# Kernel optimization log

Hardware: AMD Instinct MI355X
Metric: run time of the kernel (lower is better)

Reference implementation:

```python
import jax, jax.numpy as jnp
import numpy as np

SUB = 5      # icosphere subdivisions -> V = 10*4^5 + 2 = 10242
B = 16       # batch size
ZD = 32      # z_dim
HID = 64     # hidden_dim


def _create_icosphere(sub):
    t = (1.0 + np.sqrt(5.0)) / 2.0
    v = np.array([[-1, t, 0], [1, t, 0], [-1, -t, 0], [1, -t, 0], [0, -1, t], [0, 1, t],
                  [0, -1, -t], [0, 1, -t], [t, 0, -1], [t, 0, 1], [-t, 0, -1], [-t, 0, 1]],
                 dtype=np.float32)
    v /= np.linalg.norm(v[0])
    f = np.array([[0, 11, 5], [0, 5, 1], [0, 1, 7], [0, 7, 10], [0, 10, 11], [1, 5, 9],
                  [5, 11, 4], [11, 10, 2], [10, 7, 6], [7, 1, 8], [3, 9, 4], [3, 4, 2],
                  [3, 2, 6], [3, 6, 8], [3, 8, 9], [4, 9, 5], [2, 4, 11], [6, 2, 10],
                  [8, 6, 7], [9, 8, 1]], dtype=np.int64)
    for _ in range(sub):
        mid = {}
        nv = list(v)
        nf = []
        def gm(i1, i2):
            k = (min(i1, i2), max(i1, i2))
            if k not in mid:
                m = (v[i1] + v[i2]) / 2.0
                m = m / np.linalg.norm(m)
                mid[k] = len(nv)
                nv.append(m)
            return mid[k]
        for v0, v1, v2 in f:
            a, b, c = gm(v0, v1), gm(v1, v2), gm(v2, v0)
            nf.extend([[v0, a, c], [v1, b, a], [v2, c, b], [a, b, c]])
        v = np.array(nv, dtype=np.float32)
        f = np.array(nf, dtype=np.int64)
    return v, f


def _adjacency(faces, nv):
    # symmetric edges + self loops, sym-normalized: 1/sqrt(deg[r]*deg[c])
    e = set()
    for a, b, c in faces:
        e.update([(int(a), int(b)), (int(b), int(a)), (int(b), int(c)),
                  (int(c), int(b)), (int(c), int(a)), (int(a), int(c))])
    for i in range(nv):
        e.add((i, i))
    e = np.array(sorted(e), dtype=np.int64)
    row, col = e[:, 0], e[:, 1]
    deg = np.bincount(row, minlength=nv).astype(np.float32)
    vals = (1.0 / np.sqrt(deg[row] * deg[col])).astype(np.float32)
    return row.astype(np.int32), col.astype(np.int32), vals


def _lin(key, din, dout):
    W = jax.random.normal(key, (dout, din), jnp.float32) / np.sqrt(din)
    b = jnp.zeros((dout,), jnp.float32)
    return W, b


def setup_inputs() -> dict:
    verts, faces = _create_icosphere(SUB)
    V = len(verts)
    row, col, vals = _adjacency(faces, V)
    template = jnp.asarray(verts)

    key = jax.random.key(0)
    ks = jax.random.split(key, 16)
    # input meshes = template + small deformation (realistic for this VAE)
    x = template[None] + 0.05 * jax.random.normal(ks[0], (B, V, 3), jnp.float32)
    eps = jax.random.normal(ks[1], (B, ZD), jnp.float32)

    W1, b1 = _lin(ks[2], 3, HID)
    W2, b2 = _lin(ks[3], HID, HID)
    W3, b3 = _lin(ks[4], HID, 2 * HID)
    Wfc, bfc = _lin(ks[5], 2 * HID, 4 * HID)
    Wmu, bmu = _lin(ks[6], 4 * HID, ZD)
    Wlv, blv = _lin(ks[7], 4 * HID, ZD)
    DH = 2 * HID  # decoder hidden_dim = 128
    Wd1, bd1 = _lin(ks[8], ZD + 3, DH)
    Wd2, bd2 = _lin(ks[9], DH, DH)
    Wd3, bd3 = _lin(ks[10], DH, DH // 2)
    Wd4, bd4 = _lin(ks[11], DH // 2, 3)

    return {"x": x, "eps": eps, "row": jnp.asarray(row), "col": jnp.asarray(col),
            "vals": jnp.asarray(vals), "template": template,
            "W1": W1, "b1": b1, "W2": W2, "b2": b2, "W3": W3, "b3": b3,
            "Wfc": Wfc, "bfc": bfc, "Wmu": Wmu, "bmu": bmu, "Wlv": Wlv, "blv": blv,
            "Wd1": Wd1, "bd1": bd1, "Wd2": Wd2, "bd2": bd2,
            "Wd3": Wd3, "bd3": bd3, "Wd4": Wd4, "bd4": bd4}


def _spmm(row, col, vals, h):
    # batched sparse (V,V) @ (B,V,C): out[b,r] = sum_e vals[e] * h[b, col[e]]
    msg = h[:, col, :] * vals[None, :, None]            # (B, E, C)
    return jnp.zeros(h.shape, h.dtype).at[:, row, :].add(msg)


def _linear(x, W, b):
    return x @ W.T + b


def reference(x, eps, row, col, vals, template,
              W1, b1, W2, b2, W3, b3, Wfc, bfc, Wmu, bmu, Wlv, blv,
              Wd1, bd1, Wd2, bd2, Wd3, bd3, Wd4, bd4):
    # --- encoder: 3 graph convs (linear -> spmm -> relu), mean pool, fc ---
    h = jax.nn.relu(_spmm(row, col, vals, _linear(x, W1, b1)))
    h = jax.nn.relu(_spmm(row, col, vals, _linear(h, W2, b2)))
    h = jax.nn.relu(_spmm(row, col, vals, _linear(h, W3, b3)))
    g = h.mean(axis=1)                                   # (B, 2*HID)
    feat = jax.nn.relu(_linear(g, Wfc, bfc))             # (B, 4*HID)
    mu = _linear(feat, Wmu, bmu)                         # (B, ZD)
    log_var = jnp.clip(_linear(feat, Wlv, blv), -20.0, 20.0)
    # --- reparameterize (eps supplied as input for determinism) ---
    z = mu + eps * jnp.exp(0.5 * log_var)
    # --- decoder MLP on [z, template] per vertex (dropout = eval mode) ---
    Bn, V = x.shape[0], template.shape[0]
    z_exp = jnp.broadcast_to(z[:, None, :], (Bn, V, z.shape[-1]))
    t_exp = jnp.broadcast_to(template[None], (Bn, V, 3))
    hd = jnp.concatenate([z_exp, t_exp], axis=-1)        # (B, V, ZD+3)
    hd = jax.nn.relu(_linear(hd, Wd1, bd1))
    hd = jax.nn.relu(_linear(hd, Wd2, bd2))
    hd = jax.nn.relu(_linear(hd, Wd3, bd3))
    offsets = _linear(hd, Wd4, bd4)                      # (B, V, 3)
    recon = template[None] + offsets
    return recon, mu, log_var
```

## Files before the change

### kernel.cpp

```cpp
#include <hip/hip_runtime.h>
#include <hip/hip_bf16.h>

typedef __attribute__((ext_vector_type(8))) unsigned short ushort8;
typedef __attribute__((ext_vector_type(4))) unsigned short ushort4v;
typedef __attribute__((ext_vector_type(8))) short short8v;
typedef __attribute__((ext_vector_type(4))) float f32x4;

__device__ __forceinline__ float bf2f(unsigned short u){
  union { unsigned int i; float f; } x; x.i = ((unsigned int)u) << 16; return x.f;
}
__device__ __forceinline__ unsigned short f2bf(float f){
  __hip_bfloat16 h = __float2bfloat16(f);
  return *reinterpret_cast<unsigned short*>(&h);
}

__device__ __forceinline__ void sw_decode(int p, int NB, int& b, int& off){
  int xcd = p & 7, q = p >> 3;
  int hi = (q >= NB) ? 1 : 0;
  b = xcd + (hi << 3);
  off = q - (hi ? NB : 0);
}

__global__ void prep_k(const int* __restrict__ row, const int* __restrict__ colx,
                       const float* __restrict__ vals, int nnz,
                       int* __restrict__ col8, float* __restrict__ val8,
                       float* __restrict__ dvec, float* __restrict__ g, int V, int GN){
  int v = blockIdx.x*256 + threadIdx.x;
  if (v < GN) g[v] = 0.f;
  if (v >= V) return;
  int lo = 0, hi = nnz;
  while (lo < hi){ int m = (lo+hi)>>1; if (row[m] < v) lo = m+1; else hi = m; }
  int e0 = lo;
  int lo2 = e0; hi = nnz;
  while (lo2 < hi){ int m = (lo2+hi)>>1; if (row[m] < v+1) lo2 = m+1; else hi = m; }
  int e1 = lo2;
  float s = 0.f;
  #pragma unroll
  for (int i=0;i<8;i++){
    int e = e0 + i;
    int c  = (e < e1) ? colx[e] : 0;
    float wv = (e < e1) ? vals[e] : 0.f;
    col8[v*8+i] = c; val8[v*8+i] = wv; s += wv;
  }
  dvec[v] = s;
}

__device__ __forceinline__ void load_nbr(const int* __restrict__ col8,
    const float* __restrict__ val8, int v, int* cols, float* vv){
  int4 ca = *reinterpret_cast<const int4*>(col8 + v*8);
  int4 cb = *reinterpret_cast<const int4*>(col8 + v*8 + 4);
  float4 va = *reinterpret_cast<const float4*>(val8 + v*8);
  float4 vb = *reinterpret_cast<const float4*>(val8 + v*8 + 4);
  cols[0]=ca.x; cols[1]=ca.y; cols[2]=ca.z; cols[3]=ca.w;
  cols[4]=cb.x; cols[5]=cb.y; cols[6]=cb.z;
  vv[0]=va.x; vv[1]=va.y; vv[2]=va.z; vv[3]=va.w;
  vv[4]=vb.x; vv[5]=vb.y; vv[6]=vb.z;
}

__global__ void spmm_lin1_k(const float* __restrict__ x, const int* __restrict__ col8,
    const float* __restrict__ val8, const float* __restrict__ d,
    const float* __restrict__ W1, const float* __restrict__ b1,
    unsigned short* __restrict__ out, int V, int NB){
  __shared__ float sW[192];
  __shared__ float sB[64];
  int tid = threadIdx.x;
  if (tid < 192) sW[tid] = W1[tid];
  if (tid < 64)  sB[tid] = b1[tid];
  __syncthreads();
  int b, off; sw_decode(blockIdx.x, NB, b, off);
  int v = off*256 + tid;
  if (v >= V) return;
  const float* xb = x + (size_t)b*V*3;
  int   cs[7]; float ws[7];
  load_nbr(col8, val8, v, cs, ws);
  float s0=0.f, s1=0.f, s2=0.f;
  #pragma unroll
  for (int i=0;i<7;i++){
    const float* xr = xb + (size_t)cs[i]*3;
    s0 += ws[i]*xr[0]; s1 += ws[i]*xr[1]; s2 += ws[i]*xr[2];
  }
  float dv = d[v];
  unsigned short* orow = out + ((size_t)b*V + v)*64;
  #pragma unroll
  for (int cg=0; cg<8; ++cg){
    ushort8 o;
    #pragma unroll
    for (int k=0;k<8;k++){
      int c = cg*8 + k;
      float acc = dv*sB[c] + s0*sW[c*3] + s1*sW[c*3+1] + s2*sW[c*3+2];
      o[k] = f2bf(fmaxf(acc, 0.f));
    }
    *reinterpret_cast<ushort8*>(orow + cg*8) = o;
  }
}

__global__ __launch_bounds__(256) void spmm8s_k(const unsigned short* __restrict__ in,
    unsigned short* __restrict__ out, const int* __restrict__ col8,
    const float* __restrict__ val8, int V, int NB){
  int b, off; sw_decode(blockIdx.x, NB, b, off);
  int j = off*256 + (int)threadIdx.x;
  if (j >= V*8) return;
  int cg = j & 7; int v = j >> 3;
  const unsigned short* base = in + (size_t)b*V*64 + cg*8;
  int cols[7]; float vv[7];
  load_nbr(col8, val8, v, cols, vv);
  ushort8 g[7];
  #pragma unroll
  for (int i=0;i<7;i++) g[i] = *reinterpret_cast<const ushort8*>(base + (size_t)cols[i]*64);
  float acc[8];
  #pragma unroll
  for (int k=0;k<8;k++) acc[k] = 0.f;
  #pragma unroll
  for (int i=0;i<7;i++){
    float s = vv[i];
    #pragma unroll
    for (int k=0;k<8;k++) acc[k] += s*bf2f(g[i][k]);
  }
  ushort8 o;
  #pragma unroll
  for (int k=0;k<8;k++) o[k] = f2bf(acc[k]);
  *reinterpret_cast<ushort8*>(out + ((size_t)b*V + v)*64 + cg*8) = o;
}

template<int K, int N, bool RELU>
__global__ __launch_bounds__(256) void lin_mfma_k(const unsigned short* __restrict__ in,
    const float* __restrict__ W, const float* __restrict__ bias,
    unsigned short* __restrict__ out, const float* __restrict__ dvec, int V, int NB){
  constexpr int KP = K + 8;
  constexpr int NF = N / 16;
  constexpr int KS = K / 32;
  __shared__ unsigned short sW[N * KP];
  __shared__ float sB[N];
  int tid = threadIdx.x;
  for (int i = tid*4; i < N*K; i += 1024){
    const float4 wv = *reinterpret_cast<const float4*>(W + i);
    int n = i / K, k = i - n*K;
    unsigned short* dst = &sW[n*KP + k];
    dst[0] = f2bf(wv.x); dst[1] = f2bf(wv.y); dst[2] = f2bf(wv.z); dst[3] = f2bf(wv.w);
  }
  if (tid < N) sB[tid] = bias[tid];
  __syncthreads();

  int b, off; sw_decode(blockIdx.x, NB, b, off);
  const int wave = tid >> 6, lane = tid & 63;
  const int l15 = lane & 15, lg = lane >> 4;
  const int vbase = off*128 + wave*32;

  int v0r = vbase + l15, v1r = vbase + 16 + l15;
  int v0c = min(v0r, V-1), v1c = min(v1r, V-1);
  const size_t bb = (size_t)b*V;
  const unsigned short* bp0 = in + (bb + v0c)*K + lg*8;
  const unsigned short* bp1 = in + (bb + v1c)*K + lg*8;
  const unsigned short* aBase = &sW[l15*KP + lg*8];

  f32x4 acc[NF][2];
  #pragma unroll
  for (int nf=0; nf<NF; ++nf){ acc[nf][0] = (f32x4)0.f; acc[nf][1] = (f32x4)0.f; }

  #pragma unroll
  for (int ks=0; ks<KS; ++ks){
    short8v b0 = *reinterpret_cast<const short8v*>(bp0 + ks*32);
    short8v b1 = *reinterpret_cast<const short8v*>(bp1 + ks*32);
    #pragma unroll
    for (int nf=0; nf<NF; ++nf){
      short8v a = *reinterpret_cast<const short8v*>(aBase + nf*16*KP + ks*32);
      acc[nf][0] = __builtin_amdgcn_mfma_f32_16x16x32_bf16(a, b0, acc[nf][0], 0,0,0);
      acc[nf][1] = __builtin_amdgcn_mfma_f32_16x16x32_bf16(a, b1, acc[nf][1], 0,0,0);
    }
  }

  float d0 = dvec[v0c], d1 = dvec[v1c];
  #pragma unroll
  for (int rr=0; rr<2; ++rr){
    int v = rr ? v1r : v0r;
    if (v >= V) continue;
    float ds = rr ? d1 : d0;
    #pragma unroll
    for (int nf=0; nf<NF; ++nf){
      int nb = nf*16 + lg*4;
      ushort4v o;
      #pragma unroll
      for (int reg=0; reg<4; ++reg){
        float val = acc[nf][rr][reg] + ds*sB[nb + reg];
        if (RELU) val = val > 0.f ? val : 0.f;
        o[reg] = f2bf(val);
      }
      *reinterpret_cast<ushort4v*>(out + (bb + v)*N + nb) = o;
    }
  }
}

__global__ __launch_bounds__(256) void lin3_mean_k(const unsigned short* __restrict__ in,
    const float* __restrict__ W, const float* __restrict__ bias,
    const float* __restrict__ dvec, float* __restrict__ g, int V, int NB){
  constexpr int K = 64, N = 128, KP = K + 8, NF = N/16, KS = K/32;
  __shared__ unsigned short sW[N * KP];
  __shared__ float sB[N];
  __shared__ float gPart[128];
  int tid = threadIdx.x;
  for (int i = tid*4; i < N*K; i += 1024){
    const float4 wv = *reinterpret_cast<const float4*>(W + i);
    int n = i / K, k = i - n*K;
    unsigned short* dst = &sW[n*KP + k];
    dst[0] = f2bf(wv.x); dst[1] = f2bf(wv.y); dst[2] = f2bf(wv.z); dst[3] = f2bf(wv.w);
  }
  if (tid < N) sB[tid] = bias[tid];
  if (tid < 128) gPart[tid] = 0.f;
  __syncthreads();

  int b, off; sw_decode(blockIdx.x, NB, b, off);
  const int wave = tid >> 6, lane = tid & 63;
  const int l15 = lane & 15, lg = lane >> 4;
  const int vbase = off*128 + wave*32;

  int v0r = vbase + l15, v1r = vbase + 16 + l15;
  int v0c = min(v0r, V-1), v1c = min(v1r, V-1);
  const size_t bb = (size_t)b*V;
  const unsigned short* bp0 = in + (bb + v0c)*K + lg*8;
  const unsigned short* bp1 = in + (bb + v1c)*K + lg*8;
  const unsigned short* aBase = &sW[l15*KP + lg*8];

  f32x4 acc[NF][2];
  #pragma unroll
  for (int nf=0; nf<NF; ++nf){ acc[nf][0] = (f32x4)0.f; acc[nf][1] = (f32x4)0.f; }

  #pragma unroll
  for (int ks=0; ks<KS; ++ks){
    short8v b0 = *reinterpret_cast<const short8v*>(bp0 + ks*32);
    short8v b1 = *reinterpret_cast<const short8v*>(bp1 + ks*32);
    #pragma unroll
    for (int nf=0; nf<NF; ++nf){
      short8v a = *reinterpret_cast<const short8v*>(aBase + nf*16*KP + ks*32);
      acc[nf][0] = __builtin_amdgcn_mfma_f32_16x16x32_bf16(a, b0, acc[nf][0], 0,0,0);
      acc[nf][1] = __builtin_amdgcn_mfma_f32_16x16x32_bf16(a, b1, acc[nf][1], 0,0,0);
    }
  }

  bool ok0 = v0r < V, ok1 = v1r < V;
  float d0 = dvec[v0c], d1 = dvec[v1c];
  #pragma unroll
  for (int nf=0; nf<NF; ++nf){
    #pragma unroll
    for (int reg=0; reg<4; ++reg){
      int c = nf*16 + lg*4 + reg;
      float v0f = fmaxf(acc[nf][0][reg] + d0*sB[c], 0.f);
      float v1f = fmaxf(acc[nf][1][reg] + d1*sB[c], 0.f);
      float sA = (ok0 ? v0f : 0.f) + (ok1 ? v1f : 0.f);
      #pragma unroll
      for (int m=1; m<16; m<<=1) sA += __shfl_xor(sA, m);
      if (l15 == 0) atomicAdd(&gPart[c], sA);
    }
  }
  __syncthreads();
  if (tid < 128){
    float a = gPart[tid];
    if (a != 0.f) atomicAdd(&g[b*128 + tid], a);
  }
}

__global__ __launch_bounds__(256) void head2_k(const float* __restrict__ g,
    const float* __restrict__ Wfc, const float* __restrict__ bfc,
    const float* __restrict__ Wmu, const float* __restrict__ bmu,
    const float* __restrict__ Wlv, const float* __restrict__ blv,
    const float* __restrict__ eps, const float* __restrict__ Wd1,
    const float* __restrict__ bd1, float* __restrict__ mu_out,
    float* __restrict__ lv_out, float* __restrict__ zp, float invV){
  int b = blockIdx.x;
  int tid = threadIdx.x;
  __shared__ float sG[128];
  __shared__ float sF[256];
  __shared__ float sMu[32];
  __shared__ float sLv[32];
  __shared__ float sZ[32];
  if (tid < 128) sG[tid] = g[b*128 + tid] * invV;
  __syncthreads();
  {
    const float4* wr = reinterpret_cast<const float4*>(Wfc + tid*128);
    float acc = bfc[tid];
    #pragma unroll 8
    for (int k4=0;k4<32;k4++){
      float4 wv = wr[k4];
      acc += sG[k4*4]*wv.x + sG[k4*4+1]*wv.y + sG[k4*4+2]*wv.z + sG[k4*4+3]*wv.w;
    }
    sF[tid] = fmaxf(acc, 0.f);
  }
  __syncthreads();
  if (tid < 64){
    int c = tid & 31;
    bool isMu = tid < 32;
    const float4* wr = reinterpret_cast<const float4*>((isMu ? Wmu : Wlv) + c*256);
    float acc = isMu ? bmu[c] : blv[c];
    #pragma unroll 8
    for (int k4=0;k4<64;k4++){
      float4 wv = wr[k4];
      acc += sF[k4*4]*wv.x + sF[k4*4+1]*wv.y + sF[k4*4+2]*wv.z + sF[k4*4+3]*wv.w;
    }
    if (isMu){ sMu[c] = acc; mu_out[b*32+c] = acc; }
    else {
      acc = fminf(20.f, fmaxf(-20.f, acc));
      sLv[c] = acc; lv_out[b*32+c] = acc;
    }
  }
  __syncthreads();
  if (tid < 32) sZ[tid] = sMu[tid] + eps[b*32+tid]*expf(0.5f*sLv[tid]);
  __syncthreads();
  if (tid < 128){
    const float* wr = Wd1 + tid*35;
    float acc = bd1[tid];
    #pragma unroll
    for (int k=0;k<32;k++) acc += sZ[k]*wr[k];
    zp[b*128 + tid] = acc;
  }
}

__global__ __launch_bounds__(256) void dec_k(const float* __restrict__ zp,
    const float* __restrict__ tmpl, const float* __restrict__ Wd1,
    const float* __restrict__ Wd2, const float* __restrict__ bd2,
    const float* __restrict__ Wd3, const float* __restrict__ bd3,
    const float* __restrict__ Wd4, const float* __restrict__ bd4,
    float* __restrict__ out, int V, int NB){
  constexpr int KP = 136;
  __shared__ unsigned short sW[64*KP];
  __shared__ unsigned short sH[64*KP];
  __shared__ float sB2[128];
  __shared__ float sB3[64];
  __shared__ float sW4[192];
  __shared__ float sB4[3];
  __shared__ float sZPb[128];
  __shared__ float sWT[128*3];
  int tid = threadIdx.x;
  int b, off; sw_decode(blockIdx.x, NB, b, off);

  if (tid < 128) sB2[tid] = bd2[tid];
  if (tid < 64)  sB3[tid] = bd3[tid];
  if (tid < 192) sW4[tid] = Wd4[tid];
  if (tid < 3)   sB4[tid] = bd4[tid];
  if (tid < 128) sZPb[tid] = zp[b*128 + tid];
  if (tid < 128){
    sWT[tid*3+0] = Wd1[tid*35+32];
    sWT[tid*3+1] = Wd1[tid*35+33];
    sWT[tid*3+2] = Wd1[tid*35+34];
  }
  auto stageW = [&](const float* Wsrc){
    for (int i = tid*4; i < 64*128; i += 1024){
      float4 wv = *reinterpret_cast<const float4*>(Wsrc + i);
      int n = i >> 7, k = i & 127;
      unsigned short* dst = &sW[n*KP + k];
      dst[0]=f2bf(wv.x); dst[1]=f2bf(wv.y); dst[2]=f2bf(wv.z); dst[3]=f2bf(wv.w);
    }
  };
  stageW(Wd2);
  __syncthreads();

  const int wave = tid >> 6, lane = tid & 63;
  const int l15 = lane & 15, lg = lane >> 4;
  const int vbase = off*64 + wave*16;
  const int lrow = wave*16;

  int v0r = vbase + l15;
  int v0 = min(v0r, V-1);
  float t0x=tmpl[v0*3], t0y=tmpl[v0*3+1], t0z=tmpl[v0*3+2];

  short8v bf0[4];
  #pragma unroll
  for (int ks=0; ks<4; ++ks){
    #pragma unroll
    for (int k=0;k<8;k++){
      int c = lg*8 + ks*32 + k;
      const float* wt = &sWT[c*3];
      bf0[ks][k] = (short)f2bf(fmaxf(sZPb[c] + t0x*wt[0]+t0y*wt[1]+t0z*wt[2], 0.f));
    }
  }

  const unsigned short* aBase = &sW[l15*KP + lg*8];

  #pragma unroll
  for (int half=0; half<2; ++half){
    if (half==1){
      __syncthreads();
      stageW(Wd2 + 64*128);
      __syncthreads();
    }
    f32x4 acc[4];
    #pragma unroll
    for (int nf=0; nf<4; ++nf) acc[nf]=(f32x4)0.f;
    #pragma unroll
    for (int ks=0; ks<4; ++ks){
      #pragma unroll
      for (int nf=0; nf<4; ++nf){
        short8v a = *reinterpret_cast<const short8v*>(aBase + nf*16*KP + ks*32);
        acc[nf] = __builtin_amdgcn_mfma_f32_16x16x32_bf16(a, bf0[ks], acc[nf], 0,0,0);
      }
    }
    #pragma unroll
    for (int nf=0; nf<4; ++nf){
      int c = half*64 + nf*16 + lg*4;
      ushort4v o;
      #pragma unroll
      for (int reg=0; reg<4; ++reg)
        o[reg] = f2bf(fmaxf(acc[nf][reg] + sB2[c+reg], 0.f));
      *reinterpret_cast<ushort4v*>(&sH[(lrow + l15)*KP + c]) = o;
    }
  }
  __syncthreads();
  stageW(Wd3);
  __syncthreads();

  f32x4 acc3[4];
  #pragma unroll
  for (int nf=0; nf<4; ++nf) acc3[nf]=(f32x4)0.f;
  #pragma unroll
  for (int ks=0; ks<4; ++ks){
    short8v h0 = *reinterpret_cast<const short8v*>(&sH[(lrow + l15)*KP + ks*32 + lg*8]);
    #pragma unroll
    for (int nf=0; nf<4; ++nf){
      short8v a = *reinterpret_cast<const short8v*>(aBase + nf*16*KP + ks*32);
      acc3[nf] = __builtin_amdgcn_mfma_f32_16x16x32_bf16(a, h0, acc3[nf], 0,0,0);
    }
  }

  float p0 = 0.f, p1 = 0.f, p2 = 0.f;
  #pragma unroll
  for (int nf=0; nf<4; ++nf){
    #pragma unroll
    for (int reg=0; reg<4; ++reg){
      int c = nf*16 + lg*4 + reg;
      float h = fmaxf(acc3[nf][reg] + sB3[c], 0.f);
      p0 += h*sW4[c]; p1 += h*sW4[64+c]; p2 += h*sW4[128+c];
    }
  }
  p0 += __shfl_xor(p0,16); p0 += __shfl_xor(p0,32);
  p1 += __shfl_xor(p1,16); p1 += __shfl_xor(p1,32);
  p2 += __shfl_xor(p2,16); p2 += __shfl_xor(p2,32);
  if (lg == 0 && v0r < V){
    size_t o = ((size_t)b*V + v0r)*3;
    out[o+0] = tmpl[v0r*3+0] + p0 + sB4[0];
    out[o+1] = tmpl[v0r*3+1] + p1 + sB4[1];
    out[o+2] = tmpl[v0r*3+2] + p2 + sB4[2];
  }
}

extern "C" void kernel_launch(void* const* d_in, const int* in_sizes, int n_in,
                              void* d_out, int out_size, void* d_ws, size_t ws_size,
                              hipStream_t stream){
  const float* x    = (const float*)d_in[0];
  const float* eps  = (const float*)d_in[1];
  const int*   row  = (const int*)d_in[2];
  const int*   colx = (const int*)d_in[3];
  const float* vals = (const float*)d_in[4];
  const float* tmpl = (const float*)d_in[5];
  const float* W1 = (const float*)d_in[6];  const float* b1 = (const float*)d_in[7];
  const float* W2 = (const float*)d_in[8];  const float* b2 = (const float*)d_in[9];
  const float* W3 = (const float*)d_in[10]; const float* b3 = (const float*)d_in[11];
  const float* Wfc= (const float*)d_in[12]; const float* bfc= (const float*)d_in[13];
  const float* Wmu= (const float*)d_in[14]; const float* bmu= (const float*)d_in[15];
  const float* Wlv= (const float*)d_in[16]; const float* blv= (const float*)d_in[17];
  const float* Wd1= (const float*)d_in[18]; const float* bd1= (const float*)d_in[19];
  const float* Wd2= (const float*)d_in[20]; const float* bd2= (const float*)d_in[21];
  const float* Wd3= (const float*)d_in[22]; const float* bd3= (const float*)d_in[23];
  const float* Wd4= (const float*)d_in[24]; const float* bd4= (const float*)d_in[25];

  int V   = in_sizes[5] / 3;
  int Bn  = in_sizes[1] / 32;
  int nnz = in_sizes[2];
  int R   = Bn * V;

  char* w = (char*)d_ws;
  size_t off = 0;
  auto alloc = [&](size_t bytes)->char*{
    char* p = w + off; off = (off + bytes + 255) & ~(size_t)255; return p;
  };
  unsigned short* bufA = (unsigned short*)alloc((size_t)R * 64 * 2);
  unsigned short* bufB = (unsigned short*)alloc((size_t)R * 64 * 2);
  int*   col8 = (int*)alloc((size_t)V*8*4);
  float* val8 = (float*)alloc((size_t)V*8*4);
  float* dvec = (float*)alloc((size_t)V*4);
  float* g    = (float*)alloc((size_t)Bn*128*4);
  float* zpb  = (float*)alloc((size_t)Bn*128*4);

  float* recon  = (float*)d_out;
  float* mu_out = recon + (size_t)R*3;
  float* lv_out = mu_out + (size_t)Bn*32;

  int NB1 = (V + 255) / 256;
  int NB8 = (V*8 + 255) / 256;
  int NBm = (V + 127) / 128;
  int NBd = (V + 63) / 64;

  prep_k<<<(V+255)/256, 256, 0, stream>>>(row, colx, vals, nnz, col8, val8, dvec, g, V, Bn*128);

  spmm_lin1_k<<<16*NB1, 256, 0, stream>>>(x, col8, val8, dvec, W1, b1, bufA, V, NB1);
  spmm8s_k<<<16*NB8, 256, 0, stream>>>(bufA, bufB, col8, val8, V, NB8);
  lin_mfma_k<64,64,true><<<16*NBm, 256, 0, stream>>>(bufB, W2, b2, bufA, dvec, V, NBm);
  spmm8s_k<<<16*NB8, 256, 0, stream>>>(bufA, bufB, col8, val8, V, NB8);
  lin3_mean_k<<<16*NBm, 256, 0, stream>>>(bufB, W3, b3, dvec, g, V, NBm);

  head2_k<<<Bn, 256, 0, stream>>>(g, Wfc, bfc, Wmu, bmu, Wlv, blv, eps, Wd1, bd1,
                                  mu_out, lv_out, zpb, 1.0f/(float)V);

  dec_k<<<16*NBd, 256, 0, stream>>>(zpb, tmpl, Wd1, Wd2, bd2, Wd3, bd3, Wd4, bd4,
                                    recon, V, NBd);
}
```

Before: 132.2 us.

## Make linear and decoder kernels persistent to amortize weight staging across tiles

Three kernels (lin_mfma, lin3_mean, dec) now run as grid-stride persistent kernels with 32 blocks per batch item instead of one block per tile. Each block converts and stages its weights into shared memory once and then loops over many vertex tiles. lin3_mean accumulates pooled sums in registers across tiles before doing one shuffle-reduce and atomic pass. The decoder keeps both Wd2 and Wd3 resident in LDS, which removes the per-tile restaging and syncs but raises shared memory use and may lower occupancy.

```diff
diff --git a/kernel.cpp b/kernel.cpp
--- a/kernel.cpp
+++ b/kernel.cpp
@@ -125,7 +125,8 @@
 template<int K, int N, bool RELU>
 __global__ __launch_bounds__(256) void lin_mfma_k(const unsigned short* __restrict__ in,
     const float* __restrict__ W, const float* __restrict__ bias,
-    unsigned short* __restrict__ out, const float* __restrict__ dvec, int V, int NB){
+    unsigned short* __restrict__ out, const float* __restrict__ dvec, int V,
+    int NBLK, int NT){
   constexpr int KP = K + 8;
   constexpr int NF = N / 16;
   constexpr int KS = K / 32;
@@ -141,58 +142,60 @@
   if (tid < N) sB[tid] = bias[tid];
   __syncthreads();
 
-  int b, off; sw_decode(blockIdx.x, NB, b, off);
-  const int wave = tid >> 6, lane = tid & 63;
+  int b, off0; sw_decode(blockIdx.x, NBLK, b, off0);
+  const int lane = tid & 63, wave = tid >> 6;
   const int l15 = lane & 15, lg = lane >> 4;
-  const int vbase = off*128 + wave*32;
-
-  int v0r = vbase + l15, v1r = vbase + 16 + l15;
-  int v0c = min(v0r, V-1), v1c = min(v1r, V-1);
   const size_t bb = (size_t)b*V;
-  const unsigned short* bp0 = in + (bb + v0c)*K + lg*8;
-  const unsigned short* bp1 = in + (bb + v1c)*K + lg*8;
   const unsigned short* aBase = &sW[l15*KP + lg*8];
 
-  f32x4 acc[NF][2];
-  #pragma unroll
-  for (int nf=0; nf<NF; ++nf){ acc[nf][0] = (f32x4)0.f; acc[nf][1] = (f32x4)0.f; }
-
-  #pragma unroll
-  for (int ks=0; ks<KS; ++ks){
-    short8v b0 = *reinterpret_cast<const short8v*>(bp0 + ks*32);
-    short8v b1 = *reinterpret_cast<const short8v*>(bp1 + ks*32);
-    #pragma unroll
-    for (int nf=0; nf<NF; ++nf){
-      short8v a = *reinterpret_cast<const short8v*>(aBase + nf*16*KP + ks*32);
-      acc[nf][0] = __builtin_amdgcn_mfma_f32_16x16x32_bf16(a, b0, acc[nf][0], 0,0,0);
-      acc[nf][1] = __builtin_amdgcn_mfma_f32_16x16x32_bf16(a, b1, acc[nf][1], 0,0,0);
-    }
-  }
-
-  float d0 = dvec[v0c], d1 = dvec[v1c];
-  #pragma unroll
-  for (int rr=0; rr<2; ++rr){
-    int v = rr ? v1r : v0r;
-    if (v >= V) continue;
-    float ds = rr ? d1 : d0;
-    #pragma unroll
-    for (int nf=0; nf<NF; ++nf){
-      int nb = nf*16 + lg*4;
-      ushort4v o;
-      #pragma unroll
-      for (int reg=0; reg<4; ++reg){
-        float val = acc[nf][rr][reg] + ds*sB[nb + reg];
-        if (RELU) val = val > 0.f ? val : 0.f;
-        o[reg] = f2bf(val);
-      }
-      *reinterpret_cast<ushort4v*>(out + (bb + v)*N + nb) = o;
+  for (int off = off0; off < NT; off += NBLK){
+    const int vbase = off*128 + wave*32;
+    int v0r = vbase + l15, v1r = vbase + 16 + l15;
+    int v0c = min(v0r, V-1), v1c = min(v1r, V-1);
+    const unsigned short* bp0 = in + (bb + v0c)*K + lg*8;
+    const unsigned short* bp1 = in + (bb + v1c)*K + lg*8;
+
+    f32x4 acc[NF][2];
+    #pragma unroll
+    for (int nf=0; nf<NF; ++nf){ acc[nf][0] = (f32x4)0.f; acc[nf][1] = (f32x4)0.f; }
+
+    #pragma unroll
+    for (int ks=0; ks<KS; ++ks){
+      short8v b0 = *reinterpret_cast<const short8v*>(bp0 + ks*32);
+      short8v b1 = *reinterpret_cast<const short8v*>(bp1 + ks*32);
+      #pragma unroll
+      for (int nf=0; nf<NF; ++nf){
+        short8v a = *reinterpret_cast<const short8v*>(aBase + nf*16*KP + ks*32);
+        acc[nf][0] = __builtin_amdgcn_mfma_f32_16x16x32_bf16(a, b0, acc[nf][0], 0,0,0);
+        acc[nf][1] = __builtin_amdgcn_mfma_f32_16x16x32_bf16(a, b1, acc[nf][1], 0,0,0);
+      }
+    }
+
+    float d0 = dvec[v0c], d1 = dvec[v1c];
+    #pragma unroll
+    for (int rr=0; rr<2; ++rr){
+      int v = rr ? v1r : v0r;
+      if (v >= V) continue;
+      float ds = rr ? d1 : d0;
+      #pragma unroll
+      for (int nf=0; nf<NF; ++nf){
+        int nb = nf*16 + lg*4;
+        ushort4v o;
+        #pragma unroll
+        for (int reg=0; reg<4; ++reg){
+          float val = acc[nf][rr][reg] + ds*sB[nb + reg];
+          if (RELU) val = val > 0.f ? val : 0.f;
+          o[reg] = f2bf(val);
+        }
+        *reinterpret_cast<ushort4v*>(out + (bb + v)*N + nb) = o;
+      }
     }
   }
 }
 
 __global__ __launch_bounds__(256) void lin3_mean_k(const unsigned short* __restrict__ in,
     const float* __restrict__ W, const float* __restrict__ bias,
-    const float* __restrict__ dvec, float* __restrict__ g, int V, int NB){
+    const float* __restrict__ dvec, float* __restrict__ g, int V, int NBLK, int NT){
   constexpr int K = 64, N = 128, KP = K + 8, NF = N/16, KS = K/32;
   __shared__ unsigned short sW[N * KP];
   __shared__ float sB[N];
@@ -208,44 +211,61 @@
   if (tid < 128) gPart[tid] = 0.f;
   __syncthreads();
 
-  int b, off; sw_decode(blockIdx.x, NB, b, off);
-  const int wave = tid >> 6, lane = tid & 63;
+  int b, off0; sw_decode(blockIdx.x, NBLK, b, off0);
+  const int lane = tid & 63, wave = tid >> 6;
   const int l15 = lane & 15, lg = lane >> 4;
-  const int vbase = off*128 + wave*32;
-
-  int v0r = vbase + l15, v1r = vbase + 16 + l15;
-  int v0c = min(v0r, V-1), v1c = min(v1r, V-1);
   const size_t bb = (size_t)b*V;
-  const unsigned short* bp0 = in + (bb + v0c)*K + lg*8;
-  const unsigned short* bp1 = in + (bb + v1c)*K + lg*8;
   const unsigned short* aBase = &sW[l15*KP + lg*8];
 
-  f32x4 acc[NF][2];
-  #pragma unroll
-  for (int nf=0; nf<NF; ++nf){ acc[nf][0] = (f32x4)0.f; acc[nf][1] = (f32x4)0.f; }
-
-  #pragma unroll
-  for (int ks=0; ks<KS; ++ks){
-    short8v b0 = *reinterpret_cast<const short8v*>(bp0 + ks*32);
-    short8v b1 = *reinterpret_cast<const short8v*>(bp1 + ks*32);
+  float racc[NF][4];
+  #pragma unroll
+  for (int nf=0;nf<NF;++nf)
+    #pragma unroll
+    for (int reg=0;reg<4;++reg) racc[nf][reg] = 0.f;
+
+  for (int off = off0; off < NT; off += NBLK){
+    const int vbase = off*128 + wave*32;
+    int v0r = vbase + l15, v1r = vbase + 16 + l15;
+    int v0c = min(v0r, V-1), v1c = min(v1r, V-1);
+    const unsigned short* bp0 = in + (bb + v0c)*K + lg*8;
+    const unsigned short* bp1 = in + (bb + v1c)*K + lg*8;
+
+    f32x4 acc[NF][2];
+    #pragma unroll
+    for (int nf=0; nf<NF; ++nf){ acc[nf][0] = (f32x4)0.f; acc[nf][1] = (f32x4)0.f; }
+
+    #pragma unroll
+    for (int ks=0; ks<KS; ++ks){
+      short8v b0 = *reinterpret_cast<const short8v*>(bp0 + ks*32);
+      short8v b1 = *reinterpret_cast<const short8v*>(bp1 + ks*32);
+      #pragma unroll
+      for (int nf=0; nf<NF; ++nf){
+        short8v a = *reinterpret_cast<const short8v*>(aBase + nf*16*KP + ks*32);
+        acc[nf][0] = __builtin_amdgcn_mfma_f32_16x16x32_bf16(a, b0, acc[nf][0], 0,0,0);
+        acc[nf][1] = __builtin_amdgcn_mfma_f32_16x16x32_bf16(a, b1, acc[nf][1], 0,0,0);
+      }
+    }
+
+    bool ok0 = v0r < V, ok1 = v1r < V;
+    float d0 = dvec[v0c], d1 = dvec[v1c];
     #pragma unroll
     for (int nf=0; nf<NF; ++nf){
-      short8v a = *reinterpret_cast<const short8v*>(aBase + nf*16*KP + ks*32);
-      acc[nf][0] = __builtin_amdgcn_mfma_f32_16x16x32_bf16(a, b0, acc[nf][0], 0,0,0);
-      acc[nf][1] = __builtin_amdgcn_mfma_f32_16x16x32_bf16(a, b1, acc[nf][1], 0,0,0);
-    }
-  }
-
-  bool ok0 = v0r < V, ok1 = v1r < V;
-  float d0 = dvec[v0c], d1 = dvec[v1c];
+      #pragma unroll
+      for (int reg=0; reg<4; ++reg){
+        int c = nf*16 + lg*4 + reg;
+        float v0f = fmaxf(acc[nf][0][reg] + d0*sB[c], 0.f);
+        float v1f = fmaxf(acc[nf][1][reg] + d1*sB[c], 0.f);
+        racc[nf][reg] += (ok0 ? v0f : 0.f) + (ok1 ? v1f : 0.f);
+      }
+    }
+  }
+
   #pragma unroll
   for (int nf=0; nf<NF; ++nf){
     #pragma unroll
     for (int reg=0; reg<4; ++reg){
       int c = nf*16 + lg*4 + reg;
-      float v0f = fmaxf(acc[nf][0][reg] + d0*sB[c], 0.f);
-      float v1f = fmaxf(acc[nf][1][reg] + d1*sB[c], 0.f);
-      float sA = (ok0 ? v0f : 0.f) + (ok1 ? v1f : 0.f);
+      float sA = racc[nf][reg];
       #pragma unroll
       for (int m=1; m<16; m<<=1) sA += __shfl_xor(sA, m);
       if (l15 == 0) atomicAdd(&gPart[c], sA);
@@ -318,125 +338,120 @@
     const float* __restrict__ Wd2, const float* __restrict__ bd2,
     const float* __restrict__ Wd3, const float* __restrict__ bd3,
     const float* __restrict__ Wd4, const float* __restrict__ bd4,
-    float* __restrict__ out, int V, int NB){
+    float* __restrict__ out, int V, int NBLK, int NT){
   constexpr int KP = 136;
-  __shared__ unsigned short sW[64*KP];
+  __shared__ unsigned short sW2[128*KP];
+  __shared__ unsigned short sW3[64*KP];
   __shared__ unsigned short sH[64*KP];
   __shared__ float sB2[128];
   __shared__ float sB3[64];
   __shared__ float sW4[192];
-  __shared__ float sB4[3];
+  __shared__ float sB4v[4];
   __shared__ float sZPb[128];
   __shared__ float sWT[128*3];
   int tid = threadIdx.x;
-  int b, off; sw_decode(blockIdx.x, NB, b, off);
+  int b, off0; sw_decode(blockIdx.x, NBLK, b, off0);
 
   if (tid < 128) sB2[tid] = bd2[tid];
   if (tid < 64)  sB3[tid] = bd3[tid];
   if (tid < 192) sW4[tid] = Wd4[tid];
-  if (tid < 3)   sB4[tid] = bd4[tid];
+  if (tid < 3)   sB4v[tid] = bd4[tid];
   if (tid < 128) sZPb[tid] = zp[b*128 + tid];
   if (tid < 128){
     sWT[tid*3+0] = Wd1[tid*35+32];
     sWT[tid*3+1] = Wd1[tid*35+33];
     sWT[tid*3+2] = Wd1[tid*35+34];
   }
-  auto stageW = [&](const float* Wsrc){
-    for (int i = tid*4; i < 64*128; i += 1024){
-      float4 wv = *reinterpret_cast<const float4*>(Wsrc + i);
-      int n = i >> 7, k = i & 127;
-      unsigned short* dst = &sW[n*KP + k];
-      dst[0]=f2bf(wv.x); dst[1]=f2bf(wv.y); dst[2]=f2bf(wv.z); dst[3]=f2bf(wv.w);
-    }
-  };
-  stageW(Wd2);
+  for (int i = tid*4; i < 128*128; i += 1024){
+    float4 wv = *reinterpret_cast<const float4*>(Wd2 + i);
+    int n = i >> 7, k = i & 127;
+    unsigned short* dst = &sW2[n*KP + k];
+    dst[0]=f2bf(wv.x); dst[1]=f2bf(wv.y); dst[2]=f2bf(wv.z); dst[3]=f2bf(wv.w);
+  }
+  for (int i = tid*4; i < 64*128; i += 1024){
+    float4 wv = *reinterpret_cast<const float4*>(Wd3 + i);
+    int n = i >> 7, k = i & 127;
+    unsigned short* dst = &sW3[n*KP + k];
+    dst[0]=f2bf(wv.x); dst[1]=f2bf(wv.y); dst[2]=f2bf(wv.z); dst[3]=f2bf(wv.w);
+  }
   __syncthreads();
 
   const int wave = tid >> 6, lane = tid & 63;
   const int l15 = lane & 15, lg = lane >> 4;
-  const int vbase = off*64 + wave*16;
   const int lrow = wave*16;
-
-  int v0r = vbase + l15;
-  int v0 = min(v0r, V-1);
-  float t0x=tmpl[v0*3], t0y=tmpl[v0*3+1], t0z=tmpl[v0*3+2];
-
-  short8v bf0[4];
-  #pragma unroll
-  for (int ks=0; ks<4; ++ks){
-    #pragma unroll
-    for (int k=0;k<8;k++){
-      int c = lg*8 + ks*32 + k;
-      const float* wt = &sWT[c*3];
-      bf0[ks][k] = (short)f2bf(fmaxf(sZPb[c] + t0x*wt[0]+t0y*wt[1]+t0z*wt[2], 0.f));
-    }
-  }
-
-  const unsigned short* aBase = &sW[l15*KP + lg*8];
-
-  #pragma unroll
-  for (int half=0; half<2; ++half){
-    if (half==1){
-      __syncthreads();
-      stageW(Wd2 + 64*128);
-      __syncthreads();
-    }
-    f32x4 acc[4];
-    #pragma unroll
-    for (int nf=0; nf<4; ++nf) acc[nf]=(f32x4)0.f;
+  const unsigned short* a2Base = &sW2[l15*KP + lg*8];
+  const unsigned short* a3Base = &sW3[l15*KP + lg*8];
+
+  for (int off = off0; off < NT; off += NBLK){
+    const int vbase = off*64 + wave*16;
+    int v0r = vbase + l15;
+    int v0 = min(v0r, V-1);
+    float t0x=tmpl[v0*3], t0y=tmpl[v0*3+1], t0z=tmpl[v0*3+2];
+
+    short8v bf0[4];
     #pragma unroll
     for (int ks=0; ks<4; ++ks){
       #pragma unroll
-      for (int nf=0; nf<4; ++nf){
-        short8v a = *reinterpret_cast<const short8v*>(aBase + nf*16*KP + ks*32);
+      for (int k=0;k<8;k++){
+        int c = lg*8 + ks*32 + k;
+        const float* wt = &sWT[c*3];
+        bf0[ks][k] = (short)f2bf(fmaxf(sZPb[c] + t0x*wt[0]+t0y*wt[1]+t0z*wt[2], 0.f));
+      }
+    }
+
+    f32x4 acc[8];
+    #pragma unroll
+    for (int nf=0; nf<8; ++nf) acc[nf]=(f32x4)0.f;
+    #pragma unroll
+    for (int ks=0; ks<4; ++ks){
+      #pragma unroll
+      for (int nf=0; nf<8; ++nf){
+        short8v a = *reinterpret_cast<const short8v*>(a2Base + nf*16*KP + ks*32);
         acc[nf] = __builtin_amdgcn_mfma_f32_16x16x32_bf16(a, bf0[ks], acc[nf], 0,0,0);
       }
     }
     #pragma unroll
-    for (int nf=0; nf<4; ++nf){
-      int c = half*64 + nf*16 + lg*4;
+    for (int nf=0; nf<8; ++nf){
+      int c = nf*16 + lg*4;
       ushort4v o;
       #pragma unroll
       for (int reg=0; reg<4; ++reg)
         o[reg] = f2bf(fmaxf(acc[nf][reg] + sB2[c+reg], 0.f));
       *reinterpret_cast<ushort4v*>(&sH[(lrow + l15)*KP + c]) = o;
     }
-  }
-  __syncthreads();
-  stageW(Wd3);
-  __syncthreads();
-
-  f32x4 acc3[4];
-  #pragma unroll
-  for (int nf=0; nf<4; ++nf) acc3[nf]=(f32x4)0.f;
-  #pragma unroll
-  for (int ks=0; ks<4; ++ks){
-    short8v h0 = *reinterpret_cast<const short8v*>(&sH[(lrow + l15)*KP + ks*32 + lg*8]);
+
+    f32x4 acc3[4];
+    #pragma unroll
+    for (int nf=0; nf<4; ++nf) acc3[nf]=(f32x4)0.f;
+    #pragma unroll
+    for (int ks=0; ks<4; ++ks){
+      short8v h0 = *reinterpret_cast<const short8v*>(&sH[(lrow + l15)*KP + ks*32 + lg*8]);
+      #pragma unroll
+      for (int nf=0; nf<4; ++nf){
+        short8v a = *reinterpret_cast<const short8v*>(a3Base + nf*16*KP + ks*32);
+        acc3[nf] = __builtin_amdgcn_mfma_f32_16x16x32_bf16(a, h0, acc3[nf], 0,0,0);
+      }
+    }
+
+    float p0 = 0.f, p1 = 0.f, p2 = 0.f;
     #pragma unroll
     for (int nf=0; nf<4; ++nf){
-      short8v a = *reinterpret_cast<const short8v*>(aBase + nf*16*KP + ks*32);
-      acc3[nf] = __builtin_amdgcn_mfma_f32_16x16x32_bf16(a, h0, acc3[nf], 0,0,0);
-    }
-  }
-
-  float p0 = 0.f, p1 = 0.f, p2 = 0.f;
-  #pragma unroll
-  for (int nf=0; nf<4; ++nf){
-    #pragma unroll
-    for (int reg=0; reg<4; ++reg){
-      int c = nf*16 + lg*4 + reg;
-      float h = fmaxf(acc3[nf][reg] + sB3[c], 0.f);
-      p0 += h*sW4[c]; p1 += h*sW4[64+c]; p2 += h*sW4[128+c];
-    }
-  }
-  p0 += __shfl_xor(p0,16); p0 += __shfl_xor(p0,32);
-  p1 += __shfl_xor(p1,16); p1 += __shfl_xor(p1,32);
-  p2 += __shfl_xor(p2,16); p2 += __shfl_xor(p2,32);
-  if (lg == 0 && v0r < V){
-    size_t o = ((size_t)b*V + v0r)*3;
-    out[o+0] = tmpl[v0r*3+0] + p0 + sB4[0];
-    out[o+1] = tmpl[v0r*3+1] + p1 + sB4[1];
-    out[o+2] = tmpl[v0r*3+2] + p2 + sB4[2];
+      #pragma unroll
+      for (int reg=0; reg<4; ++reg){
+        int c = nf*16 + lg*4 + reg;
+        float h = fmaxf(acc3[nf][reg] + sB3[c], 0.f);
+        p0 += h*sW4[c]; p1 += h*sW4[64+c]; p2 += h*sW4[128+c];
+      }
+    }
+    p0 += __shfl_xor(p0,16); p0 += __shfl_xor(p0,32);
+    p1 += __shfl_xor(p1,16); p1 += __shfl_xor(p1,32);
+    p2 += __shfl_xor(p2,16); p2 += __shfl_xor(p2,32);
+    if (lg == 0 && v0r < V){
+      size_t o = ((size_t)b*V + v0r)*3;
+      out[o+0] = tmpl[v0r*3+0] + p0 + sB4v[0];
+      out[o+1] = tmpl[v0r*3+1] + p1 + sB4v[1];
+      out[o+2] = tmpl[v0r*3+2] + p2 + sB4v[2];
+    }
   }
 }
 
@@ -484,20 +499,21 @@
 
   int NB1 = (V + 255) / 256;
   int NB8 = (V*8 + 255) / 256;
-  int NBm = (V + 127) / 128;
-  int NBd = (V + 63) / 64;
+  int NTm = (V + 127) / 128;
+  int NTd = (V + 63) / 64;
+  int NBLK = 32;
 
   prep_k<<<(V+255)/256, 256, 0, stream>>>(row, colx, vals, nnz, col8, val8, dvec, g, V, Bn*128);
 
   spmm_lin1_k<<<16*NB1, 256, 0, stream>>>(x, col8, val8, dvec, W1, b1, bufA, V, NB1);
   spmm8s_k<<<16*NB8, 256, 0, stream>>>(bufA, bufB, col8, val8, V, NB8);
-  lin_mfma_k<64,64,true><<<16*NBm, 256, 0, stream>>>(bufB, W2, b2, bufA, dvec, V, NBm);
+  lin_mfma_k<64,64,true><<<16*NBLK, 256, 0, stream>>>(bufB, W2, b2, bufA, dvec, V, NBLK, NTm);
   spmm8s_k<<<16*NB8, 256, 0, stream>>>(bufA, bufB, col8, val8, V, NB8);
-  lin3_mean_k<<<16*NBm, 256, 0, stream>>>(bufB, W3, b3, dvec, g, V, NBm);
+  lin3_mean_k<<<16*NBLK, 256, 0, stream>>>(bufB, W3, b3, dvec, g, V, NBLK, NTm);
 
   head2_k<<<Bn, 256, 0, stream>>>(g, Wfc, bfc, Wmu, bmu, Wlv, blv, eps, Wd1, bd1,
                                   mu_out, lv_out, zpb, 1.0f/(float)V);
 
-  dec_k<<<16*NBd, 256, 0, stream>>>(zpb, tmpl, Wd1, Wd2, bd2, Wd3, bd3, Wd4, bd4,
-                                    recon, V, NBd);
-}
+  dec_k<<<16*NBLK, 256, 0, stream>>>(zpb, tmpl, Wd1, Wd2, bd2, Wd3, bd3, Wd4, bd4,
+                                     recon, V, NBLK, NTd);
+}
```

Measured after the change: 126.2 us, median of 2. 1.05x faster.
